# Optimization experiments

Hardware: AMD Instinct MI355X
Metric: run time of the kernel (lower is better)

The kernel has to match this reference:

```python
import jax, jax.numpy as jnp
import numpy as np

ITERS = 2
EPS = 1e-6

_OFFSETS = [(a, b, c) for a in (-1, 0, 1) for b in (-1, 0, 1) for c in (-1, 0, 1)]


def _erosion_step(im):
    # product over full 3x3x3 neighborhood (connectivity=26 -> all 27 voxels),
    # out-of-bounds padded with 1 (identity for product)
    B, C, D, H, W = im.shape
    p = jnp.pad(im, ((0, 0), (0, 0), (1, 1), (1, 1), (1, 1)), constant_values=1.0)
    prod = jnp.ones_like(im)
    for dz, dy, dx in _OFFSETS:
        prod = prod * p[:, :, 1 + dz:1 + dz + D, 1 + dy:1 + dy + H, 1 + dx:1 + dx + W]
    return prod


def _distance_map(im, iters=ITERS):
    # PositiveDistanceMap: dils = -SoftErosion3D(1-im) where SoftErosion3D
    # returns temp = -sum_k im_k (im_0 = 1-im, im_{k+1} = im_k * erosion(im_k))
    cur = 1.0 - im
    acc = jnp.zeros_like(cur)
    for _ in range(iters):
        acc = acc + cur
        cur = cur * _erosion_step(cur)
    return acc


def _lah_loss(x, y_onehot):
    axes = (2, 3, 4)  # batch_lah=False -> per (batch, class) reduction
    dm_hat = _distance_map(x)
    dm_gt = _distance_map(y_onehot)
    fp = (dm_gt * x).sum(axes)
    fn = (dm_hat * y_onehot).sum(axes)
    # norm == 0
    fp = fp / (x.sum(axes) + EPS)
    fn = fn / (y_onehot.sum(axes) + EPS)
    lah = (fp + fn + jnp.abs(fp - fn)) / 2  # logsum2 == elementwise max
    return lah[:, 1:].mean()  # do_bg=False drops background channel


def setup_inputs() -> dict:
    key = jax.random.key(0)
    k1, k2 = jax.random.split(key)
    x = jax.random.uniform(k1, (2, 4, 128, 128, 128), dtype=jnp.float32)
    y = jax.random.randint(k2, (2, 1, 128, 128, 128), 0, 4, dtype=jnp.int64)
    return {"x": x, "y": y}


def reference(x, y):
    C = x.shape[1]
    y_onehot = jax.nn.one_hot(y[:, 0], C, axis=1, dtype=x.dtype)  # [B,C,D,H,W]
    return _lah_loss(x, y_onehot)
```

## Files before the change

### kernel.cpp

```cpp
#include <hip/hip_runtime.h>

constexpr int SPB = 1 << 21;
constexpr float EPSV = 1e-6f;

__device__ unsigned char g_mask[2 * SPB];

constexpr int K0_ZSEG = 4;
constexpr int K0_NBLK = (2 * (128 / K0_ZSEG) * 128) / 4;

struct MEnt { int pk, cx, cy; };

__device__ __forceinline__ MEnt k0_load(const int* __restrict__ yb, int s,
                                        int rbase0, bool ym1, bool yp1) {
    MEnt e;
    const int rb = (s << 14) | rbase0;
    int2 vc = *(const int2*)(yb + rb);
    int nib0 = 1 << vc.x, nib1 = 1 << vc.y;
    if (ym1) { int2 vm = *(const int2*)(yb + rb - 128); nib0 |= 1 << vm.x; nib1 |= 1 << vm.y; }
    if (yp1) { int2 vp = *(const int2*)(yb + rb + 128); nib0 |= 1 << vp.x; nib1 |= 1 << vp.y; }
    e.pk = nib0 | (nib1 << 8);
    e.cx = vc.x; e.cy = vc.y;
    return e;
}

__global__ __launch_bounds__(256) void mask_build(const int* __restrict__ y32) {
    const int wid = (blockIdx.x << 2) | (threadIdx.x >> 6);
    const int lane = threadIdx.x & 63;
    const int yy = wid & 127;
    const int zs = (wid >> 7) & 31;
    const int b = (wid >> 12) & 1;
    const int x0 = lane << 1;
    const int z0 = zs * K0_ZSEG;
    const bool ym1 = yy > 0, yp1 = yy < 127;
    const int rbase0 = (yy << 7) | x0;

    const int* __restrict__ yb = y32 + ((long)b << 21);
    unsigned char* __restrict__ mb = g_mask + ((long)b << 21);

    MEnt e0, e1;
    if (z0 > 0) e0 = k0_load(yb, z0 - 1, rbase0, ym1, yp1);
    else { e0.pk = 0; e0.cx = 0; e0.cy = 0; }
    e1 = k0_load(yb, z0, rbase0, ym1, yp1);

#pragma unroll
    for (int dz = 0; dz < K0_ZSEG; ++dz) {
        const int z = z0 + dz;
        MEnt e2;
        if (z + 1 < 128) e2 = k0_load(yb, z + 1, rbase0, ym1, yp1);
        else { e2.pk = 0; e2.cx = 0; e2.cy = 0; }

        const int zor = e0.pk | e1.pk | e2.pk;
        int orL = __shfl_up(zor, 1);
        if (lane == 0) orL = 0;
        int orR = __shfl_down(zor, 1);
        if (lane == 63) orR = 0;
        const int full0 = (zor | (zor >> 8) | (orL >> 8)) & 15;
        const int full1 = (zor | (zor >> 8) | orR) & 15;

        const unsigned short st =
            (unsigned short)((full0 | (e1.cx << 4)) | ((full1 | (e1.cy << 4)) << 8));
        *(unsigned short*)(mb + ((z << 14) | rbase0)) = st;

        e0 = e1; e1 = e2;
    }
}

constexpr int ZC = 8;
constexpr int NBLK = 8 * 16 * (128 / ZC);

__global__ __launch_bounds__(256) void lah_main(const float* __restrict__ x,
                                                float* __restrict__ acc) {
    __shared__ float raw[3][10][128];
    __shared__ float sred[4];

    const int bid = blockIdx.x;
    const int plane = bid & 7;
    const int b = plane >> 2, cls = plane & 3;
    const int inner = bid >> 3;
    const int yc = inner & 15;
    const int zq = inner >> 4;
    const int r0 = yc * 8;
    const int z0 = zq * ZC;
    const int t = threadIdx.x;
    const int rr = t >> 5;
    const int xc = (t & 31) << 2;
    const int lane = t & 63;

    const float* __restrict__ xp = x + ((long)plane << 21);
    const unsigned char* __restrict__ mb = g_mask + ((long)b << 21);
    const int mrow = (r0 + rr) << 7;

    auto gload = [&](int k, int i) -> float4 {
        const int gr = r0 - 1 + i;
        if ((unsigned)k > 127u || (unsigned)gr > 127u)
            return make_float4(0.f, 0.f, 0.f, 0.f);
        return *(const float4*)(xp + ((k << 14) | (gr << 7) | xc));
    };
    auto stage_direct = [&](int k, int s) {
        *(float4*)&raw[s][rr][xc] = gload(k, rr);
        if (t < 64) *(float4*)&raw[s][8 + (t >> 5)][xc] = gload(k, 8 + (t >> 5));
    };
    auto yprod = [&](int s, float4& cx) -> float4 {
        const float4 a = *(const float4*)&raw[s][rr][xc];
        const float4 bq = *(const float4*)&raw[s][rr + 1][xc];
        const float4 c = *(const float4*)&raw[s][rr + 2][xc];
        cx = bq;
        float4 o;
        o.x = (1.f - a.x) * (1.f - bq.x) * (1.f - c.x);
        o.y = (1.f - a.y) * (1.f - bq.y) * (1.f - c.y);
        o.z = (1.f - a.z) * (1.f - bq.z) * (1.f - c.z);
        o.w = (1.f - a.w) * (1.f - bq.w) * (1.f - c.w);
        return o;
    };

    stage_direct(z0 - 1, 0);
    stage_direct(z0, 1);
    stage_direct(z0 + 1, 2);
    __syncthreads();
    float4 cxd, cx0;
    float4 ypm1 = yprod(0, cxd);
    float4 yp0 = yprod(1, cx0);
    unsigned mcur = *(const unsigned*)(mb + ((z0 << 14) | mrow | xc));

    int sm = 0, s0 = 1, sp = 2;

    float fp = 0.f, fn = 0.f, sx = 0.f, sy = 0.f;

#pragma unroll
    for (int dz = 0; dz < ZC; ++dz) {
        const int z = z0 + dz;
        __syncthreads();

        float4 gA = make_float4(0.f, 0.f, 0.f, 0.f);
        float4 gB = make_float4(0.f, 0.f, 0.f, 0.f);
        unsigned mnext = 0;
        if (dz < ZC - 1) {
            gA = gload(z + 2, rr);
            if (t < 64) gB = gload(z + 2, 8 + (t >> 5));
            mnext = *(const unsigned*)(mb + (((z + 1) << 14) | mrow | xc));
        }

        float4 cx1;
        const float4 ypp1 = yprod(sp, cx1);

        {
            const float zp0 = ypm1.x * yp0.x * ypp1.x;
            const float zp1 = ypm1.y * yp0.y * ypp1.y;
            const float zp2 = ypm1.z * yp0.z * ypp1.z;
            const float zp3 = ypm1.w * yp0.w * ypp1.w;
            float zl = __shfl_up(zp3, 1);
            if ((t & 31) == 0) zl = 1.f;
            float zr = __shfl_down(zp0, 1);
            if ((t & 31) == 31) zr = 1.f;
            const float t01 = zp0 * zp1, t12 = zp1 * zp2, t23 = zp2 * zp3;
            const float P[4] = {zl * t01, t01 * zp2, t12 * zp3, t23 * zr};
            const float xa[4] = {cx0.x, cx0.y, cx0.z, cx0.w};
#pragma unroll
            for (int j = 0; j < 4; ++j) {
                const int m = (mcur >> (j * 8)) & 0xFF;
                const bool pres = (m >> cls) & 1;
                const bool eq = (m >> 4) == cls;
                const float xv = xa[j];
                sx += xv;
                fp += eq ? 0.f : xv * (pres ? 1.f : 2.f);
                fn += eq ? (1.f - xv) * (1.f + P[j]) : 0.f;
                sy += eq ? 1.f : 0.f;
            }
        }

        if (dz < ZC - 1) {
            *(float4*)&raw[sm][rr][xc] = gA;
            if (t < 64) *(float4*)&raw[sm][8 + (t >> 5)][xc] = gB;
        }

        const int tmp = sm; sm = s0; s0 = sp; sp = tmp;
        ypm1 = yp0; yp0 = ypp1; cx0 = cx1; mcur = mnext;
    }

    float rr4[4] = {fp, fn, sx, sy};
#pragma unroll
    for (int i = 0; i < 4; ++i) {
        float vv = rr4[i];
#pragma unroll
        for (int off = 32; off >= 1; off >>= 1) vv += __shfl_down(vv, off);
        rr4[i] = vv;
    }
    if (t < 4) sred[t] = 0.f;
    __syncthreads();
    if (lane == 0) {
#pragma unroll
        for (int i = 0; i < 4; ++i) atomicAdd(&sred[i], rr4[i]);
    }
    __syncthreads();
    if (t < 4)
        atomicAdd(&acc[b * 16 + t * 4 + cls], sred[t]);
}

__global__ void lah_finalize(const float* __restrict__ acc, float* __restrict__ out) {
    float loss = 0.f;
#pragma unroll
    for (int b = 0; b < 2; ++b) {
#pragma unroll
        for (int c = 1; c < 4; ++c) {
            const float fp = acc[b * 16 + 0 + c];
            const float fn = acc[b * 16 + 4 + c];
            const float sxv = acc[b * 16 + 8 + c];
            const float syv = acc[b * 16 + 12 + c];
            loss += fmaxf(fp / (sxv + EPSV), fn / (syv + EPSV));
        }
    }
    out[0] = loss / 6.f;
}

extern "C" void kernel_launch(void* const* d_in, const int* in_sizes, int n_in,
                              void* d_out, int out_size, void* d_ws, size_t ws_size,
                              hipStream_t stream) {
    const float* x = (const float*)d_in[0];
    const int* y32 = (const int*)d_in[1];
    float* out = (float*)d_out;
    float* acc = (float*)d_ws;

    hipMemsetAsync(d_ws, 0, 32 * sizeof(float), stream);
    mask_build<<<K0_NBLK, 256, 0, stream>>>(y32);
    lah_main<<<NBLK, 256, 0, stream>>>(x, acc);
    lah_finalize<<<1, 1, 0, stream>>>(acc, out);
}
```

Before: 50.60 us.

## Deepen z-plane prefetch pipeline with four-slot shared ring buffer

Shared staging grows from three to four z-slices, indexed by z mod 4. Global loads are now issued two planes ahead and held in registers for one extra iteration. The single barrier moves after the shared store, so global-load latency has more independent work to hide behind. The cost is more registers and more shared memory per block, which may reduce occupancy.

```diff
diff --git a/kernel.cpp b/kernel.cpp
--- a/kernel.cpp
+++ b/kernel.cpp
@@ -70,7 +70,7 @@
 
 __global__ __launch_bounds__(256) void lah_main(const float* __restrict__ x,
                                                 float* __restrict__ acc) {
-    __shared__ float raw[3][10][128];
+    __shared__ float raw[4][10][128];
     __shared__ float sred[4];
 
     const int bid = blockIdx.x;
@@ -85,10 +85,13 @@
     const int rr = t >> 5;
     const int xc = (t & 31) << 2;
     const int lane = t & 63;
+    const int xrow = 8 + (t >> 5);
 
     const float* __restrict__ xp = x + ((long)plane << 21);
     const unsigned char* __restrict__ mb = g_mask + ((long)b << 21);
     const int mrow = (r0 + rr) << 7;
+
+    const float4 Z4 = make_float4(0.f, 0.f, 0.f, 0.f);
 
     auto gload = [&](int k, int i) -> float4 {
         const int gr = r0 - 1 + i;
@@ -96,9 +99,10 @@
             return make_float4(0.f, 0.f, 0.f, 0.f);
         return *(const float4*)(xp + ((k << 14) | (gr << 7) | xc));
     };
-    auto stage_direct = [&](int k, int s) {
+    auto stage_direct = [&](int k) {
+        const int s = k & 3;
         *(float4*)&raw[s][rr][xc] = gload(k, rr);
-        if (t < 64) *(float4*)&raw[s][8 + (t >> 5)][xc] = gload(k, 8 + (t >> 5));
+        if (t < 64) *(float4*)&raw[s][xrow][xc] = gload(k, xrow);
     };
     auto yprod = [&](int s, float4& cx) -> float4 {
         const float4 a = *(const float4*)&raw[s][rr][xc];
@@ -113,35 +117,34 @@
         return o;
     };
 
-    stage_direct(z0 - 1, 0);
-    stage_direct(z0, 1);
-    stage_direct(z0 + 1, 2);
+    stage_direct(z0 - 1);
+    stage_direct(z0);
+    stage_direct(z0 + 1);
+    float4 pA = gload(z0 + 2, rr);
+    float4 pB = (t < 64) ? gload(z0 + 2, xrow) : Z4;
     __syncthreads();
     float4 cxd, cx0;
-    float4 ypm1 = yprod(0, cxd);
-    float4 yp0 = yprod(1, cx0);
+    float4 ypm1 = yprod((z0 - 1) & 3, cxd);
+    float4 yp0 = yprod(z0 & 3, cx0);
     unsigned mcur = *(const unsigned*)(mb + ((z0 << 14) | mrow | xc));
-
-    int sm = 0, s0 = 1, sp = 2;
 
     float fp = 0.f, fn = 0.f, sx = 0.f, sy = 0.f;
 
 #pragma unroll
     for (int dz = 0; dz < ZC; ++dz) {
         const int z = z0 + dz;
-        __syncthreads();
-
-        float4 gA = make_float4(0.f, 0.f, 0.f, 0.f);
-        float4 gB = make_float4(0.f, 0.f, 0.f, 0.f);
+
+        float4 nA = Z4, nB = Z4;
+        if (dz <= ZC - 3) {
+            nA = gload(z + 3, rr);
+            if (t < 64) nB = gload(z + 3, xrow);
+        }
         unsigned mnext = 0;
-        if (dz < ZC - 1) {
-            gA = gload(z + 2, rr);
-            if (t < 64) gB = gload(z + 2, 8 + (t >> 5));
+        if (dz <= ZC - 2)
             mnext = *(const unsigned*)(mb + (((z + 1) << 14) | mrow | xc));
-        }
 
         float4 cx1;
-        const float4 ypp1 = yprod(sp, cx1);
+        const float4 ypp1 = yprod((z + 1) & 3, cx1);
 
         {
             const float zp0 = ypm1.x * yp0.x * ypp1.x;
@@ -168,12 +171,14 @@
             }
         }
 
-        if (dz < ZC - 1) {
-            *(float4*)&raw[sm][rr][xc] = gA;
-            if (t < 64) *(float4*)&raw[sm][8 + (t >> 5)][xc] = gB;
-        }
-
-        const int tmp = sm; sm = s0; s0 = sp; sp = tmp;
+        if (dz <= ZC - 2) {
+            const int s = (z + 2) & 3;
+            *(float4*)&raw[s][rr][xc] = pA;
+            if (t < 64) *(float4*)&raw[s][xrow][xc] = pB;
+        }
+        __syncthreads();
+
+        pA = nA; pB = nB;
         ypm1 = yp0; yp0 = ypp1; cx0 = cx1; mcur = mnext;
     }
 
```

Result: faster. 49.22 us (-2.7%).
